# Kernel tuning notes

Measured on AMD Instinct MI355X. Metric: run time of the kernel, lower is better.

## Reference

```python
import jax, jax.numpy as jnp
import numpy as np

TEMPERATURE = 0.5
EPS = 1e-8  # torch.nn.CosineSimilarity default eps


def setup_inputs() -> dict:
    key = jax.random.key(0)
    k1, k2 = jax.random.split(key)
    B, D = 4096, 256
    z1 = jax.random.normal(k1, (B, D), dtype=jnp.float32)
    # z2 = perturbed view of z1 so positive cosine sims are positive
    # (original torch code takes log of the RAW cosine sim, which is NaN
    #  for negative positives; realistic SimCLR positives are correlated views)
    z2 = z1 + 0.1 * jax.random.normal(k2, (B, D), dtype=jnp.float32)
    return {"z1": z1, "z2": z2}


def reference(z1, z2):
    B = z1.shape[0]
    z = jnp.concatenate([z1, z2], axis=0)                      # [2B, D]
    norm = jnp.maximum(jnp.linalg.norm(z, axis=-1, keepdims=True), EPS)
    zn = z / norm
    sim = zn @ zn.T                                            # [2B, 2B] cosine sims
    # positives: sim[i, i+B] and sim[i+B, i] (RAW cosine, per original code)
    pos = jnp.concatenate([jnp.diagonal(sim, offset=B),
                           jnp.diagonal(sim, offset=-B)])      # [2B]
    # mask self-similarity diagonal to -inf before exp-sum
    diag = jnp.eye(2 * B, dtype=bool)
    sim_masked = jnp.where(diag, -jnp.inf, sim)
    denom = jnp.sum(jnp.exp(sim_masked / TEMPERATURE), axis=-1)  # [2B]
    loss = -jnp.mean(jnp.log(pos / denom))
    return loss
```

## Files before the change

### kernel.cpp

```cpp
#include <hip/hip_runtime.h>
#include <hip/hip_bf16.h>


#define NROWS 8192
#define BHALF 4096
#define DDIM  256

typedef __attribute__((ext_vector_type(4))) int   i32x4;
typedef __attribute__((ext_vector_type(8))) int   i32x8;
typedef __attribute__((ext_vector_type(4))) float f32x4;

#define SCALE1 0x7F7F7F7F
#define TWO_LOG2E 2.8853900817779268f

__device__ __forceinline__ void load_lds16(const unsigned char* g, unsigned char* l) {
    __builtin_amdgcn_global_load_lds(
        (const __attribute__((address_space(1))) void*)g,
        (__attribute__((address_space(3))) void*)l, 16, 0, 0);
}

__global__ __launch_bounds__(256) void prep_kernel(const float* __restrict__ z1,
                                                   const float* __restrict__ z2,
                                                   unsigned char* __restrict__ zn8,
                                                   float* __restrict__ posPart,
                                                   float* __restrict__ denom,
                                                   float* __restrict__ out) {
    __shared__ float sp[4];
    int wave = threadIdx.x >> 6;
    int lane = threadIdx.x & 63;
    int i    = blockIdx.x * 4 + wave;
    float4 a = reinterpret_cast<const float4*>(z1 + (size_t)i * DDIM)[lane];
    float4 b = reinterpret_cast<const float4*>(z2 + (size_t)i * DDIM)[lane];
    float ss1 = a.x * a.x + a.y * a.y + a.z * a.z + a.w * a.w;
    float ss2 = b.x * b.x + b.y * b.y + b.z * b.z + b.w * b.w;
    float dd  = a.x * b.x + a.y * b.y + a.z * b.z + a.w * b.w;
    #pragma unroll
    for (int off = 32; off; off >>= 1) {
        ss1 += __shfl_xor(ss1, off);
        ss2 += __shfl_xor(ss2, off);
        dd  += __shfl_xor(dd, off);
    }
    float n1 = fmaxf(sqrtf(ss1), 1e-8f);
    float n2 = fmaxf(sqrtf(ss2), 1e-8f);
    float i1 = 1.0f / n1, i2 = 1.0f / n2;
    int pa = __builtin_amdgcn_cvt_pk_fp8_f32(a.x * i1, a.y * i1, 0, 0);
    pa     = __builtin_amdgcn_cvt_pk_fp8_f32(a.z * i1, a.w * i1, pa, 1);
    int pb = __builtin_amdgcn_cvt_pk_fp8_f32(b.x * i2, b.y * i2, 0, 0);
    pb     = __builtin_amdgcn_cvt_pk_fp8_f32(b.z * i2, b.w * i2, pb, 1);
    reinterpret_cast<int*>(zn8 + (size_t)i * DDIM)[lane] = pa;
    reinterpret_cast<int*>(zn8 + (size_t)(i + BHALF) * DDIM)[lane] = pb;
    if (lane == 0) sp[wave] = __logf(dd * i1 * i2);
    if (threadIdx.x < 8) denom[blockIdx.x * 8 + threadIdx.x] = 0.0f;
    if (blockIdx.x == 0 && threadIdx.x == 64) out[0] = 0.0f;
    __syncthreads();
    if (threadIdx.x == 0)
        posPart[blockIdx.x] = sp[0] + sp[1] + sp[2] + sp[3];
}

__global__ __launch_bounds__(256, 2) void denom_kernel(const unsigned char* __restrict__ zn8,
                                                       float* __restrict__ denom) {
    __shared__ __align__(16) unsigned char sA[128 * DDIM];
    __shared__ __align__(16) unsigned char sB[128 * DDIM];

    int x = blockIdx.x, y = blockIdx.y;
    int bi, bj;
    if (x > y) { bi = y;      bj = x - 1;  }
    else       { bi = 63 - y; bj = 63 - x; }
    int iBase = bi * 128;
    int jBase = bj * 128;
    bool isDiag = (bi == bj);

    int t    = threadIdx.x;
    int lane = t & 63;
    int wave = t >> 6;
    int col  = lane & 15;
    int quad = lane >> 4;
    int wm = wave >> 1, wn = wave & 1;

    int rowL  = t >> 4;
    int chunk = (t & 15) ^ rowL;
    const unsigned char* gA = zn8 + (size_t)(iBase + rowL) * DDIM + chunk * 16;
    const unsigned char* gB = zn8 + (size_t)(jBase + rowL) * DDIM + chunk * 16;
    unsigned char* lA = sA + t * 16;
    unsigned char* lB = sB + t * 16;
    #pragma unroll
    for (int s = 0; s < 8; s++) {
        load_lds16(gA + s * 4096, lA + s * 4096);
        load_lds16(gB + s * 4096, lB + s * 4096);
    }
    __syncthreads();

    i32x8 bfr[4][2];
    {
        const unsigned char* bRow = sB + (size_t)(wn * 64 + col) * DDIM;
        #pragma unroll
        for (int nt = 0; nt < 4; nt++) {
            #pragma unroll
            for (int ks = 0; ks < 2; ks++) {
                int g0 = ks * 8 + quad * 2;
                i32x4 lo = *(const i32x4*)(bRow + nt * 16 * DDIM + ((g0    ) ^ col) * 16);
                i32x4 hi = *(const i32x4*)(bRow + nt * 16 * DDIM + ((g0 + 1) ^ col) * 16);
                bfr[nt][ks] = __builtin_shufflevector(lo, hi, 0, 1, 2, 3, 4, 5, 6, 7);
            }
        }
    }

    float rs[4][4];
    float cs[4] = {0.f, 0.f, 0.f, 0.f};
    #pragma unroll
    for (int mt = 0; mt < 4; mt++)
        #pragma unroll
        for (int r = 0; r < 4; r++) rs[mt][r] = 0.f;

    const unsigned char* aRow = sA + (size_t)(wm * 64 + col) * DDIM;
    #pragma unroll
    for (int mt = 0; mt < 4; mt++) {
        i32x8 af[2];
        #pragma unroll
        for (int ks = 0; ks < 2; ks++) {
            int g0 = ks * 8 + quad * 2;
            i32x4 lo = *(const i32x4*)(aRow + mt * 16 * DDIM + ((g0    ) ^ col) * 16);
            i32x4 hi = *(const i32x4*)(aRow + mt * 16 * DDIM + ((g0 + 1) ^ col) * 16);
            af[ks] = __builtin_shufflevector(lo, hi, 0, 1, 2, 3, 4, 5, 6, 7);
        }
        int gi = iBase + wm * 64 + mt * 16;
        #pragma unroll
        for (int nt = 0; nt < 4; nt++) {
            f32x4 acc = {0.f, 0.f, 0.f, 0.f};
            acc = __builtin_amdgcn_mfma_scale_f32_16x16x128_f8f6f4(
                      af[0], bfr[nt][0], acc, 0, 0, 0, SCALE1, 0, SCALE1);
            acc = __builtin_amdgcn_mfma_scale_f32_16x16x128_f8f6f4(
                      af[1], bfr[nt][1], acc, 0, 0, 0, SCALE1, 0, SCALE1);
            bool dtile = (gi == jBase + wn * 64 + nt * 16);
            float csl = 0.f;
            #pragma unroll
            for (int r = 0; r < 4; r++) {
                float e = exp2f(acc[r] * TWO_LOG2E);
                if (dtile && (quad * 4 + r) == col) e = 0.f;
                rs[mt][r] += e;
                csl += e;
            }
            cs[nt] += csl;
        }
    }

    if (!isDiag) {
        #pragma unroll
        for (int nt = 0; nt < 4; nt++) {
            float v = cs[nt];
            v += __shfl_xor(v, 16);
            v += __shfl_xor(v, 32);
            if (quad == 0)
                atomicAdd(&denom[jBase + wn * 64 + nt * 16 + col], v);
        }
    }

    #pragma unroll
    for (int mt = 0; mt < 4; mt++)
        #pragma unroll
        for (int r = 0; r < 4; r++) {
            float v = rs[mt][r];
            v += __shfl_xor(v, 1);
            v += __shfl_xor(v, 2);
            v += __shfl_xor(v, 4);
            v += __shfl_xor(v, 8);
            rs[mt][r] = v;
        }
    __syncthreads();
    float* red = (float*)sA;
    if (col == 0) {
        #pragma unroll
        for (int mt = 0; mt < 4; mt++)
            #pragma unroll
            for (int r = 0; r < 4; r++)
                red[wn * 128 + wm * 64 + mt * 16 + quad * 4 + r] = rs[mt][r];
    }
    __syncthreads();
    if (t < 128)
        atomicAdd(&denom[iBase + t], red[t] + red[128 + t]);
}

__global__ __launch_bounds__(256) void loss_kernel(const float* __restrict__ posPart,
                                                   const float* __restrict__ denom,
                                                   float* __restrict__ out) {
    __shared__ float sdata[4];
    int t = threadIdx.x;
    float s = __logf(denom[blockIdx.x * 256 + t]);
    if (t < 32) s -= 2.0f * posPart[blockIdx.x * 32 + t];
    #pragma unroll
    for (int off = 32; off; off >>= 1) s += __shfl_xor(s, off);
    if ((t & 63) == 0) sdata[t >> 6] = s;
    __syncthreads();
    if (t == 0)
        atomicAdd(out, (sdata[0] + sdata[1] + sdata[2] + sdata[3]) * (1.0f / NROWS));
}

extern "C" void kernel_launch(void* const* d_in, const int* in_sizes, int n_in,
                              void* d_out, int out_size, void* d_ws, size_t ws_size,
                              hipStream_t stream) {
    const float* z1 = (const float*)d_in[0];
    const float* z2 = (const float*)d_in[1];

    unsigned char* zn8 = (unsigned char*)d_ws;
    float* denom   = (float*)((char*)d_ws + (size_t)NROWS * DDIM);
    float* posPart = denom + NROWS;

    prep_kernel<<<BHALF / 4, 256, 0, stream>>>(z1, z2, zn8, posPart, denom, (float*)d_out);
    denom_kernel<<<dim3(65, 32), 256, 0, stream>>>(zn8, denom);
    loss_kernel<<<NROWS / 256, 256, 0, stream>>>(posPart, denom, (float*)d_out);
}
```

Baseline: 89.27 us.

## Stream B tile through double-buffered LDS chunks and raise denom kernel occupancy

The denominator kernel now keeps the A tile's MFMA fragments in registers and streams the B tile in 16-row chunks through two small LDS buffers. Each chunk is loaded while the previous one is computed. LDS use drops from 64KB to 40KB so launch bounds can request 4 blocks per CU instead of 2. Column partial sums are collected in LDS, reusing the A region, and added once per column, while row sums are added by atomics directly from each wave. The cost is eight barriers per block and the memory-wait latency that comes with them.

```diff
diff --git a/kernel.cpp b/kernel.cpp
--- a/kernel.cpp
+++ b/kernel.cpp
@@ -57,10 +57,13 @@
         posPart[blockIdx.x] = sp[0] + sp[1] + sp[2] + sp[3];
 }
 
-__global__ __launch_bounds__(256, 2) void denom_kernel(const unsigned char* __restrict__ zn8,
+__global__ __launch_bounds__(256, 4) void denom_kernel(const unsigned char* __restrict__ zn8,
                                                        float* __restrict__ denom) {
-    __shared__ __align__(16) unsigned char sA[128 * DDIM];
-    __shared__ __align__(16) unsigned char sB[128 * DDIM];
+    __shared__ __align__(16) unsigned char sMem[40960];
+    unsigned char* sA  = sMem;
+    unsigned char* sB0 = sMem + 32768;
+    unsigned char* sB1 = sMem + 36864;
+    float* colPart = (float*)sMem;
 
     int x = blockIdx.x, y = blockIdx.y;
     int bi, bj;
@@ -75,88 +78,93 @@
     int wave = t >> 6;
     int col  = lane & 15;
     int quad = lane >> 4;
-    int wm = wave >> 1, wn = wave & 1;
 
     int rowL  = t >> 4;
-    int chunk = (t & 15) ^ rowL;
-    const unsigned char* gA = zn8 + (size_t)(iBase + rowL) * DDIM + chunk * 16;
-    const unsigned char* gB = zn8 + (size_t)(jBase + rowL) * DDIM + chunk * 16;
-    unsigned char* lA = sA + t * 16;
-    unsigned char* lB = sB + t * 16;
-    #pragma unroll
-    for (int s = 0; s < 8; s++) {
-        load_lds16(gA + s * 4096, lA + s * 4096);
-        load_lds16(gB + s * 4096, lB + s * 4096);
-    }
-    __syncthreads();
-
-    i32x8 bfr[4][2];
+    int chunkA = (t & 15) ^ rowL;
+    int chunkB = (t & 15) ^ (t >> 4);
+    const unsigned char* gBbase = zn8 + (size_t)(jBase + (t >> 4)) * DDIM + chunkB * 16;
+
     {
-        const unsigned char* bRow = sB + (size_t)(wn * 64 + col) * DDIM;
-        #pragma unroll
-        for (int nt = 0; nt < 4; nt++) {
+        const unsigned char* gA = zn8 + (size_t)(iBase + rowL) * DDIM + chunkA * 16;
+        #pragma unroll
+        for (int q = 0; q < 8; q++)
+            load_lds16(gA + q * 4096, sA + t * 16 + q * 4096);
+        load_lds16(gBbase, sB0 + t * 16);
+    }
+    __syncthreads();
+
+    i32x8 af[2][2];
+    {
+        const unsigned char* aRow = sA + (size_t)(wave * 32 + col) * DDIM;
+        #pragma unroll
+        for (int mt = 0; mt < 2; mt++)
             #pragma unroll
             for (int ks = 0; ks < 2; ks++) {
                 int g0 = ks * 8 + quad * 2;
-                i32x4 lo = *(const i32x4*)(bRow + nt * 16 * DDIM + ((g0    ) ^ col) * 16);
-                i32x4 hi = *(const i32x4*)(bRow + nt * 16 * DDIM + ((g0 + 1) ^ col) * 16);
-                bfr[nt][ks] = __builtin_shufflevector(lo, hi, 0, 1, 2, 3, 4, 5, 6, 7);
+                i32x4 lo = *(const i32x4*)(aRow + mt * 16 * DDIM + ((g0    ) ^ col) * 16);
+                i32x4 hi = *(const i32x4*)(aRow + mt * 16 * DDIM + ((g0 + 1) ^ col) * 16);
+                af[mt][ks] = __builtin_shufflevector(lo, hi, 0, 1, 2, 3, 4, 5, 6, 7);
             }
-        }
-    }
-
-    float rs[4][4];
-    float cs[4] = {0.f, 0.f, 0.f, 0.f};
-    #pragma unroll
-    for (int mt = 0; mt < 4; mt++)
+    }
+    __syncthreads();
+
+    colPart[wave * 128 + lane] = 0.0f;
+    colPart[wave * 128 + 64 + lane] = 0.0f;
+
+    load_lds16(gBbase + (size_t)16 * DDIM, sB1 + t * 16);
+
+    float rs[2][4];
+    #pragma unroll
+    for (int mt = 0; mt < 2; mt++)
         #pragma unroll
         for (int r = 0; r < 4; r++) rs[mt][r] = 0.f;
 
-    const unsigned char* aRow = sA + (size_t)(wm * 64 + col) * DDIM;
-    #pragma unroll
-    for (int mt = 0; mt < 4; mt++) {
-        i32x8 af[2];
+    for (int s = 0; s < 8; s++) {
+        if (s) __syncthreads();
+
+        if (s + 1 < 8)
+            load_lds16(gBbase + (size_t)(s + 1) * 16 * DDIM,
+                       ((s + 1) & 1 ? sB1 : sB0) + t * 16);
+
+        const unsigned char* bRow = ((s & 1) ? sB1 : sB0) + (size_t)col * DDIM;
+        i32x8 bfr[2];
         #pragma unroll
         for (int ks = 0; ks < 2; ks++) {
             int g0 = ks * 8 + quad * 2;
-            i32x4 lo = *(const i32x4*)(aRow + mt * 16 * DDIM + ((g0    ) ^ col) * 16);
-            i32x4 hi = *(const i32x4*)(aRow + mt * 16 * DDIM + ((g0 + 1) ^ col) * 16);
-            af[ks] = __builtin_shufflevector(lo, hi, 0, 1, 2, 3, 4, 5, 6, 7);
-        }
-        int gi = iBase + wm * 64 + mt * 16;
-        #pragma unroll
-        for (int nt = 0; nt < 4; nt++) {
+            i32x4 lo = *(const i32x4*)(bRow + ((g0    ) ^ col) * 16);
+            i32x4 hi = *(const i32x4*)(bRow + ((g0 + 1) ^ col) * 16);
+            bfr[ks] = __builtin_shufflevector(lo, hi, 0, 1, 2, 3, 4, 5, 6, 7);
+        }
+
+        float cs = 0.f;
+        #pragma unroll
+        for (int mt = 0; mt < 2; mt++) {
+            int gi = iBase + wave * 32 + mt * 16;
             f32x4 acc = {0.f, 0.f, 0.f, 0.f};
             acc = __builtin_amdgcn_mfma_scale_f32_16x16x128_f8f6f4(
-                      af[0], bfr[nt][0], acc, 0, 0, 0, SCALE1, 0, SCALE1);
+                      af[mt][0], bfr[0], acc, 0, 0, 0, SCALE1, 0, SCALE1);
             acc = __builtin_amdgcn_mfma_scale_f32_16x16x128_f8f6f4(
-                      af[1], bfr[nt][1], acc, 0, 0, 0, SCALE1, 0, SCALE1);
-            bool dtile = (gi == jBase + wn * 64 + nt * 16);
-            float csl = 0.f;
+                      af[mt][1], bfr[1], acc, 0, 0, 0, SCALE1, 0, SCALE1);
+            bool dtile = (gi == jBase + s * 16);
             #pragma unroll
             for (int r = 0; r < 4; r++) {
                 float e = exp2f(acc[r] * TWO_LOG2E);
                 if (dtile && (quad * 4 + r) == col) e = 0.f;
                 rs[mt][r] += e;
-                csl += e;
+                cs += e;
             }
-            cs[nt] += csl;
-        }
-    }
-
-    if (!isDiag) {
-        #pragma unroll
-        for (int nt = 0; nt < 4; nt++) {
-            float v = cs[nt];
-            v += __shfl_xor(v, 16);
-            v += __shfl_xor(v, 32);
+        }
+
+        if (!isDiag) {
+            cs += __shfl_xor(cs, 16);
+            cs += __shfl_xor(cs, 32);
             if (quad == 0)
-                atomicAdd(&denom[jBase + wn * 64 + nt * 16 + col], v);
-        }
-    }
-
-    #pragma unroll
-    for (int mt = 0; mt < 4; mt++)
+                colPart[wave * 128 + s * 16 + col] = cs;
+        }
+    }
+
+    #pragma unroll
+    for (int mt = 0; mt < 2; mt++)
         #pragma unroll
         for (int r = 0; r < 4; r++) {
             float v = rs[mt][r];
@@ -164,20 +172,14 @@
             v += __shfl_xor(v, 2);
             v += __shfl_xor(v, 4);
             v += __shfl_xor(v, 8);
-            rs[mt][r] = v;
-        }
-    __syncthreads();
-    float* red = (float*)sA;
-    if (col == 0) {
-        #pragma unroll
-        for (int mt = 0; mt < 4; mt++)
-            #pragma unroll
-            for (int r = 0; r < 4; r++)
-                red[wn * 128 + wm * 64 + mt * 16 + quad * 4 + r] = rs[mt][r];
-    }
-    __syncthreads();
-    if (t < 128)
-        atomicAdd(&denom[iBase + t], red[t] + red[128 + t]);
+            if (col == 0)
+                atomicAdd(&denom[iBase + wave * 32 + mt * 16 + quad * 4 + r], v);
+        }
+
+    __syncthreads();
+    if (t < 128 && !isDiag)
+        atomicAdd(&denom[jBase + t],
+                  colPart[t] + colPart[128 + t] + colPart[256 + t] + colPart[384 + t]);
 }
 
 __global__ __launch_bounds__(256) void loss_kernel(const float* __restrict__ posPart,
```

Result: no change. 89.95 us (+0.8%).
